# Performance work log

Hardware: AMD Instinct MI355X
Metric: run time of the kernel (lower is better)

## Reference

```python
import jax, jax.numpy as jnp
import numpy as np

N_HEAD = 16
N_EMBD = 1024
TIME_EMBD = 64
EPS = 1e-5

def _ln(x, w, b):
    mu = jnp.mean(x, axis=-1, keepdims=True)
    var = jnp.mean(jnp.square(x - mu), axis=-1, keepdims=True)
    return (x - mu) * jax.lax.rsqrt(var + EPS) * w + b

def _gelu(x):
    return jax.nn.gelu(x, approximate=False)

def setup_inputs() -> dict:
    key = jax.random.key(0)
    ks = jax.random.split(key, 12)
    B, T, D, TE = 2, 2048, N_EMBD, TIME_EMBD
    C = D + TE  # 1088
    s = lambda fan_in: 1.0 / np.sqrt(fan_in)
    return {
        "z": jax.random.normal(ks[0], (B, T, D), jnp.float32),
        "t": jax.random.uniform(ks[1], (B,), jnp.float32),
        # time_mlp: Linear(1, TE) -> GELU -> Linear(TE, TE)
        "w_t1": jax.random.normal(ks[2], (1, TE), jnp.float32) * s(1),
        "b_t1": jnp.zeros((TE,), jnp.float32),
        "w_t2": jax.random.normal(ks[3], (TE, TE), jnp.float32) * s(TE),
        "b_t2": jnp.zeros((TE,), jnp.float32),
        # attention
        "ln_a_w": jnp.ones((C,), jnp.float32),
        "ln_a_b": jnp.zeros((C,), jnp.float32),
        "w_attn": jax.random.normal(ks[4], (C, 3 * D), jnp.float32) * s(C),
        "b_attn": jnp.zeros((3 * D,), jnp.float32),
        "w_proj": jax.random.normal(ks[5], (D, D), jnp.float32) * s(D),
        "b_proj": jnp.zeros((D,), jnp.float32),
        # mlp
        "ln_m_w": jnp.ones((C,), jnp.float32),
        "ln_m_b": jnp.zeros((C,), jnp.float32),
        "w_fc": jax.random.normal(ks[6], (C, 4 * D), jnp.float32) * s(C),
        "b_fc": jnp.zeros((4 * D,), jnp.float32),
        "w_fc2": jax.random.normal(ks[7], (4 * D, D), jnp.float32) * s(4 * D),
        "b_fc2": jnp.zeros((D,), jnp.float32),
    }

def reference(z, t, w_t1, b_t1, w_t2, b_t2, ln_a_w, ln_a_b, w_attn, b_attn,
              w_proj, b_proj, ln_m_w, ln_m_b, w_fc, b_fc, w_fc2, b_fc2):
    B, T, D = z.shape
    H, hd = N_HEAD, N_EMBD // N_HEAD
    # time embedding: [B, TE] broadcast over T
    t_emb = _gelu(t[:, None] @ w_t1 + b_t1) @ w_t2 + b_t2
    t_emb_bt = jnp.broadcast_to(t_emb[:, None, :], (B, T, TIME_EMBD))
    # --- attention with time-conditioned input ---
    zt = jnp.concatenate([z, t_emb_bt], axis=-1)            # [B,T,D+TE]
    x = _ln(zt, ln_a_w, ln_a_b)
    qkv = x @ w_attn + b_attn                               # [B,T,3D]
    q, k, v = jnp.split(qkv, 3, axis=-1)
    q = q.reshape(B, T, H, hd)
    k = k.reshape(B, T, H, hd)
    v = v.reshape(B, T, H, hd)
    att = jnp.einsum('bqhd,bkhd->bhqk', q, k) * (1.0 / np.sqrt(hd))
    mask = jnp.tril(jnp.ones((T, T), bool))
    att = jnp.where(mask, att, -jnp.inf)
    att = jax.nn.softmax(att, axis=-1)
    y = jnp.einsum('bhqk,bkhd->bqhd', att, v).reshape(B, T, D)
    h = y @ w_proj + b_proj                                 # [B,T,D]
    # --- mlp with time-conditioned input ---
    ht = jnp.concatenate([h, t_emb_bt], axis=-1)
    m = _ln(ht, ln_m_w, ln_m_b)
    dz = _gelu(m @ w_fc + b_fc) @ w_fc2 + b_fc2             # [B,T,D]
    return dz
```

## Files before the change

kernel.cpp:

```cpp
#include <hip/hip_runtime.h>
#include <stdint.h>
#include <math.h>

#define T_SEQ 2048
#define NHEAD 16
#define HD 64
#define DMODEL 1024
#define CDIM 1088
#define MROWS 4096

typedef uint16_t u16;
typedef __bf16 b8v __attribute__((ext_vector_type(8)));
typedef float f4v __attribute__((ext_vector_type(4)));

typedef __attribute__((address_space(3))) void lds_void;
typedef const __attribute__((address_space(1))) void glb_void;

#define GLL(g, l) __builtin_amdgcn_global_load_lds((glb_void*)(g), (lds_void*)(l), 16, 0, 0)

__device__ __forceinline__ float b2f(u16 u) {
  union { uint32_t i; float f; } c; c.i = ((uint32_t)u) << 16; return c.f;
}
__device__ __forceinline__ u16 f2b(float f) {
  union { float f; uint32_t i; } c; c.f = f;
  uint32_t x = c.i;
  return (u16)((x + 0x7fffu + ((x >> 16) & 1u)) >> 16);
}
__device__ __forceinline__ float gelu_f(float x) {
  float ax = fabsf(x);
  float xs = ax * 0.70710678118654752f;
  float t = __frcp_rn(1.0f + 0.3275911f * xs);
  float poly = ((((1.061405429f * t - 1.453152027f) * t + 1.421413741f) * t
                 - 0.284496736f) * t + 0.254829592f) * t;
  float e = __expf(-xs * xs);
  float er = 1.0f - poly * e;
  er = copysignf(er, x);
  return 0.5f * x * (1.0f + er);
}

__global__ void time_mlp_kernel(const float* __restrict__ t, const float* __restrict__ w1,
                                const float* __restrict__ b1, const float* __restrict__ w2,
                                const float* __restrict__ b2, float* __restrict__ temb) {
  __shared__ float h1[2][64];
  int tid = threadIdx.x;
  int b = tid >> 6, i = tid & 63;
  float tv = t[b];
  h1[b][i] = gelu_f(tv * w1[i] + b1[i]);
  __syncthreads();
  float acc = b2[i];
  for (int k = 0; k < 64; ++k) acc += h1[b][k] * w2[k * 64 + i];
  temb[b * 64 + i] = acc;
}

__global__ __launch_bounds__(256) void transpose_kernel(const float* __restrict__ src,
                                                        u16* __restrict__ dst,
                                                        int R, int C) {
  __shared__ u16 tile[32][33];
  int tx = threadIdx.x & 31, ty = threadIdx.x >> 5;
  int c0 = blockIdx.x * 32, r0 = blockIdx.y * 32;
#pragma unroll
  for (int i = 0; i < 4; ++i) {
    int r = ty + i * 8;
    tile[r][tx] = f2b(src[(size_t)(r0 + r) * C + c0 + tx]);
  }
  __syncthreads();
#pragma unroll
  for (int i = 0; i < 4; ++i) {
    int c = ty + i * 8;
    dst[(size_t)(c0 + c) * R + r0 + tx] = tile[tx][c];
  }
}

__global__ __launch_bounds__(256) void add4_kernel(const float4* __restrict__ a,
                                                   const float4* __restrict__ b,
                                                   const float4* __restrict__ c,
                                                   const float4* __restrict__ d,
                                                   float4* __restrict__ o, int n4) {
  int i = blockIdx.x * 256 + threadIdx.x;
  if (i < n4) {
    float4 x = a[i], y = b[i], z = c[i], w = d[i];
    o[i] = float4{x.x + y.x + z.x + w.x, x.y + y.y + z.y + w.y,
                  x.z + y.z + z.z + w.z, x.w + y.w + z.w + w.w};
  }
}

__global__ __launch_bounds__(256) void ln_concat_kernel(const float* __restrict__ zf,
                                                        const float* __restrict__ zf2,
                                                        const float* __restrict__ temb,
                                                        const float* __restrict__ w,
                                                        const float* __restrict__ bvec,
                                                        u16* __restrict__ xout,
                                                        int mode) {
  __shared__ float red[4];
  int row = blockIdx.x;
  int b = row / T_SEQ;
  int tid = threadIdx.x;
  float v[5];
  float sum = 0.f;
#pragma unroll
  for (int i = 0; i < 5; ++i) {
    int c = tid + i * 256;
    float val = 0.f;
    if (c < CDIM) {
      if (c < DMODEL) {
        size_t idx = (size_t)row * DMODEL + c;
        if (mode == 1) val = zf[idx];
        else val = zf[idx] + zf2[idx];
      } else {
        val = temb[b * 64 + (c - DMODEL)];
      }
    }
    v[i] = val;
    sum += val;
  }
#pragma unroll
  for (int off = 32; off; off >>= 1) sum += __shfl_xor(sum, off, 64);
  int wv = tid >> 6, ln = tid & 63;
  if (ln == 0) red[wv] = sum;
  __syncthreads();
  float mean = (red[0] + red[1] + red[2] + red[3]) * (1.0f / CDIM);
  __syncthreads();
  float sq = 0.f;
#pragma unroll
  for (int i = 0; i < 5; ++i) {
    int c = tid + i * 256;
    if (c < CDIM) { float d = v[i] - mean; sq += d * d; }
  }
#pragma unroll
  for (int off = 32; off; off >>= 1) sq += __shfl_xor(sq, off, 64);
  if (ln == 0) red[wv] = sq;
  __syncthreads();
  float inv = rsqrtf((red[0] + red[1] + red[2] + red[3]) * (1.0f / CDIM) + 1e-5f);
#pragma unroll
  for (int i = 0; i < 5; ++i) {
    int c = tid + i * 256;
    if (c < CDIM)
      xout[(size_t)row * CDIM + c] = f2b((v[i] - mean) * inv * w[c] + bvec[c]);
  }
}

__global__ __launch_bounds__(512, 2) void gemm256_kernel(
    const u16* __restrict__ A, const u16* __restrict__ Bt,
    const float* __restrict__ bias,
    void* __restrict__ c0, void* __restrict__ c1,
    void* __restrict__ c2, void* __restrict__ c3,
    int M, int N, int K, int k_tiles, int do_gelu, int out_f32) {
  __shared__ u16 As[2][256 * 64];
  __shared__ u16 Bs[2][256 * 64];
  const int tid = threadIdx.x;
  const int wave = tid >> 6, lane = tid & 63;
  const int wr = wave >> 2, wc = wave & 3;
  const int lrow = lane & 15, quad = lane >> 4;

  int nxy = gridDim.x * gridDim.y;
  int bid = blockIdx.y * gridDim.x + blockIdx.x;
  int cpx = nxy >> 3;
  int swz = (bid & 7) * cpx + (bid >> 3);
  int bx = swz % gridDim.x, by = swz / gridDim.x;
  const int m0 = bx * 256, n0 = by * 256;
  const int kz = blockIdx.z;
  const int kb = kz * k_tiles * 64;
  const int NT = k_tiles;

  const int sr = tid >> 3;
  const int sc = ((tid & 7) ^ ((tid >> 3) & 7)) * 8;
  const u16* gA = A + (size_t)(m0 + sr) * K + kb + sc;
  const u16* gB = Bt + (size_t)(n0 + sr) * K + kb + sc;

  f4v acc[8][4] = {};
  b8v bq[2][4];

  auto STAGE_A = [&](int t, int h) {
    const u16* g = gA + (size_t)(h * 128) * K + t * 64;
    u16* l = (u16*)As[t & 1] + h * 8192 + (wave << 9);
    GLL(g, l);
    GLL(g + (size_t)64 * K, l + 4096);
  };
  auto STAGE_B = [&](int t, int h) {
    const u16* g = gB + (size_t)(h * 128) * K + t * 64;
    u16* l = (u16*)Bs[t & 1] + h * 8192 + (wave << 9);
    GLL(g, l);
    GLL(g + (size_t)64 * K, l + 4096);
  };

  STAGE_A(0, 0); STAGE_B(0, 0); STAGE_B(0, 1);
  STAGE_A(0, 1);
  if (NT > 1) { STAGE_A(1, 0); STAGE_B(1, 0); STAGE_B(1, 1); }
  if (NT > 1) asm volatile("s_waitcnt vmcnt(8)" ::: "memory");
  else        asm volatile("s_waitcnt vmcnt(2)" ::: "memory");
  __builtin_amdgcn_s_barrier();

  for (int t = 0; t < NT; ++t) {
    const char* abase = (const char*)As[t & 1];
    const char* bbase = (const char*)Bs[t & 1];
    const int asw = (lrow & 7) << 4;
    b8v af[4];

#pragma unroll
    for (int j = 0; j < 4; ++j)
      af[j] = *(const b8v*)(abase + (j * 32 + wr * 16 + lrow) * 128 + ((quad * 16) ^ asw));
#pragma unroll
    for (int n = 0; n < 4; ++n)
      bq[0][n] = *(const b8v*)(bbase + (wc * 64 + n * 16 + lrow) * 128 + ((quad * 16) ^ asw));
    if (t + 1 < NT) STAGE_A(t + 1, 1);
    __builtin_amdgcn_s_barrier();
    __builtin_amdgcn_s_setprio(1);
#pragma unroll
    for (int j = 0; j < 4; ++j)
#pragma unroll
      for (int n = 0; n < 4; ++n)
        acc[j][n] = __builtin_amdgcn_mfma_f32_16x16x32_bf16(bq[0][n], af[j], acc[j][n], 0, 0, 0);
    __builtin_amdgcn_s_setprio(0);
    __builtin_amdgcn_s_barrier();

#pragma unroll
    for (int j = 0; j < 4; ++j)
      af[j] = *(const b8v*)(abase + (j * 32 + wr * 16 + lrow) * 128 + ((64 + quad * 16) ^ asw));
#pragma unroll
    for (int n = 0; n < 4; ++n)
      bq[1][n] = *(const b8v*)(bbase + (wc * 64 + n * 16 + lrow) * 128 + ((64 + quad * 16) ^ asw));
    __builtin_amdgcn_s_barrier();
    __builtin_amdgcn_s_setprio(1);
#pragma unroll
    for (int j = 0; j < 4; ++j)
#pragma unroll
      for (int n = 0; n < 4; ++n)
        acc[j][n] = __builtin_amdgcn_mfma_f32_16x16x32_bf16(bq[1][n], af[j], acc[j][n], 0, 0, 0);
    __builtin_amdgcn_s_setprio(0);
    if (t + 1 < NT) asm volatile("s_waitcnt vmcnt(8)" ::: "memory");
    else            asm volatile("s_waitcnt vmcnt(0)" ::: "memory");
    __builtin_amdgcn_s_barrier();

#pragma unroll
    for (int j = 0; j < 4; ++j)
      af[j] = *(const b8v*)(abase + (128 + j * 32 + wr * 16 + lrow) * 128 + ((quad * 16) ^ asw));
    if (t + 2 < NT) { STAGE_B(t + 2, 0); STAGE_A(t + 2, 0); }
    __builtin_amdgcn_s_barrier();
    __builtin_amdgcn_s_setprio(1);
#pragma unroll
    for (int j = 0; j < 4; ++j)
#pragma unroll
      for (int n = 0; n < 4; ++n)
        acc[4 + j][n] = __builtin_amdgcn_mfma_f32_16x16x32_bf16(bq[0][n], af[j], acc[4 + j][n], 0, 0, 0);
    __builtin_amdgcn_s_setprio(0);
    __builtin_amdgcn_s_barrier();

#pragma unroll
    for (int j = 0; j < 4; ++j)
      af[j] = *(const b8v*)(abase + (128 + j * 32 + wr * 16 + lrow) * 128 + ((64 + quad * 16) ^ asw));
    if (t + 2 < NT) STAGE_B(t + 2, 1);
    __builtin_amdgcn_s_barrier();
    __builtin_amdgcn_s_setprio(1);
#pragma unroll
    for (int j = 0; j < 4; ++j)
#pragma unroll
      for (int n = 0; n < 4; ++n)
        acc[4 + j][n] = __builtin_amdgcn_mfma_f32_16x16x32_bf16(bq[1][n], af[j], acc[4 + j][n], 0, 0, 0);
    __builtin_amdgcn_s_setprio(0);
    if (t + 1 < NT) {
      if (t + 2 < NT) asm volatile("s_waitcnt vmcnt(8)" ::: "memory");
      else            asm volatile("s_waitcnt vmcnt(2)" ::: "memory");
    }
    __builtin_amdgcn_s_barrier();
  }

  void* Cout = (kz == 0) ? c0 : (kz == 1) ? c1 : (kz == 2) ? c2 : c3;
#pragma unroll
  for (int mh = 0; mh < 2; ++mh)
#pragma unroll
    for (int j = 0; j < 4; ++j) {
      int grow = m0 + mh * 128 + j * 32 + wr * 16 + lrow;
      size_t rb = (size_t)grow * N;
#pragma unroll
      for (int n = 0; n < 4; ++n) {
        int gcol = n0 + wc * 64 + n * 16 + quad * 4;
        float b0 = 0.f, b1 = 0.f, b2 = 0.f, b3 = 0.f;
        if (kz == 0) {
          float4 bv = *(const float4*)(bias + gcol);
          b0 = bv.x; b1 = bv.y; b2 = bv.z; b3 = bv.w;
        }
        f4v a = acc[mh * 4 + j][n];
        float v0 = a[0] + b0, v1 = a[1] + b1, v2 = a[2] + b2, v3 = a[3] + b3;
        if (do_gelu) {
          v0 = gelu_f(v0); v1 = gelu_f(v1); v2 = gelu_f(v2); v3 = gelu_f(v3);
        }
        if (out_f32) {
          *(float4*)((float*)Cout + rb + gcol) = float4{v0, v1, v2, v3};
        } else {
          ushort4 ov;
          ov.x = f2b(v0); ov.y = f2b(v1); ov.z = f2b(v2); ov.w = f2b(v3);
          *(ushort4*)((u16*)Cout + rb + gcol) = ov;
        }
      }
    }
}

__global__ __launch_bounds__(256) void gemm_splitk2_kernel(const u16* __restrict__ A,
                                                           const u16* __restrict__ Bt,
                                                           const float* __restrict__ bias,
                                                           float* __restrict__ C0,
                                                           float* __restrict__ C1,
                                                           int M, int N, int K, int Kc) {
  __shared__ u16 As[2][128 * 32];
  __shared__ u16 Bs[2][128 * 32];
  const int tid = threadIdx.x;
  const int wave = tid >> 6, lane = tid & 63;
  const int wr = wave >> 1, wc = wave & 1;
  const int m0 = blockIdx.x * 128;
  const int n0 = blockIdx.y * 128;
  const int kz = blockIdx.z;
  const int lrow = lane & 15, quad = lane >> 4;
  const int srow = lane >> 2, sseg = lane & 3;

  const u16* gA0 = A  + (size_t)(m0 + wave * 32 + srow) * K + kz * Kc + sseg * 8;
  const u16* gA1 = gA0 + (size_t)16 * K;
  const u16* gB0 = Bt + (size_t)(n0 + wave * 32 + srow) * K + kz * Kc + sseg * 8;
  const u16* gB1 = gB0 + (size_t)16 * K;
  const int la0 = (wave * 32) * 32, la1 = (wave * 32 + 16) * 32;

  f4v acc[4][4] = {};

  GLL(gA0, &As[0][la0]); GLL(gA1, &As[0][la1]);
  GLL(gB0, &Bs[0][la0]); GLL(gB1, &Bs[0][la1]);

  int cur = 0;
  for (int k0 = 0; k0 < Kc; k0 += 32) {
    __syncthreads();
    if (k0 + 32 < Kc) {
      int nxt = cur ^ 1;
      GLL(gA0 + k0 + 32, &As[nxt][la0]); GLL(gA1 + k0 + 32, &As[nxt][la1]);
      GLL(gB0 + k0 + 32, &Bs[nxt][la0]); GLL(gB1 + k0 + 32, &Bs[nxt][la1]);
    }
    b8v af[4], bfr[4];
#pragma unroll
    for (int mi = 0; mi < 4; ++mi)
      af[mi] = *(const b8v*)(&As[cur][(wr * 64 + mi * 16 + lrow) * 32 + quad * 8]);
#pragma unroll
    for (int ni = 0; ni < 4; ++ni)
      bfr[ni] = *(const b8v*)(&Bs[cur][(wc * 64 + ni * 16 + lrow) * 32 + quad * 8]);
#pragma unroll
    for (int mi = 0; mi < 4; ++mi)
#pragma unroll
      for (int ni = 0; ni < 4; ++ni)
        acc[mi][ni] = __builtin_amdgcn_mfma_f32_16x16x32_bf16(bfr[ni], af[mi], acc[mi][ni], 0, 0, 0);
    cur ^= 1;
  }

  float* C = kz ? C1 : C0;
#pragma unroll
  for (int mi = 0; mi < 4; ++mi) {
    int grow = m0 + wr * 64 + mi * 16 + lrow;
    size_t rb = (size_t)grow * N;
#pragma unroll
    for (int ni = 0; ni < 4; ++ni) {
      int gcol = n0 + wc * 64 + ni * 16 + quad * 4;
      float b0 = 0.f, b1 = 0.f, b2 = 0.f, b3 = 0.f;
      if (kz == 0) {
        float4 bv = *(const float4*)(bias + gcol);
        b0 = bv.x; b1 = bv.y; b2 = bv.z; b3 = bv.w;
      }
      *(float4*)(C + rb + gcol) = float4{acc[mi][ni][0] + b0, acc[mi][ni][1] + b1,
                                         acc[mi][ni][2] + b2, acc[mi][ni][3] + b3};
    }
  }
}

__global__ __launch_bounds__(256) void attn_mfma_kernel(const u16* __restrict__ qkv,
                                                        u16* __restrict__ y) {
  __shared__ u16 Ks[64 * 72];
  __shared__ u16 Vts[64 * 72];
  __shared__ u16 Ps[64 * 72];
  const int bh = blockIdx.x;
  const int b = bh >> 4, h = bh & 15;
  const int qt = 31 - blockIdx.y;
  const int tid = threadIdx.x, w = tid >> 6, lane = tid & 63;
  const int lrow = lane & 15, quad = lane >> 4;
  const int q0 = qt * 64;
  const int qg = q0 + w * 16 + lrow;

  b8v qf[2];
#pragma unroll
  for (int dc = 0; dc < 2; ++dc)
    qf[dc] = *(const b8v*)(qkv + (size_t)(b * T_SEQ + qg) * 3072 + h * 64 + dc * 32 + quad * 8);

  f4v oacc[4] = {};
  float mrun = -__builtin_inff(), lrun = 0.f;

  const int nch = qt + 1;
  for (int ct = 0; ct < nch; ++ct) {
    __syncthreads();
    {
      int r = tid >> 2, sg = tid & 3;
      const u16* src = qkv + (size_t)(b * T_SEQ + ct * 64 + r) * 3072 + h * 64 + 1024 + sg * 16;
      *(uint4*)(&Ks[r * 72 + sg * 16]) = *(const uint4*)(src);
      *(uint4*)(&Ks[r * 72 + sg * 16 + 8]) = *(const uint4*)(src + 8);
    }
    {
      int pr = tid >> 3, dsg = tid & 7;
      const u16* v0 = qkv + (size_t)(b * T_SEQ + ct * 64 + 2 * pr) * 3072 + h * 64 + 2048 + dsg * 8;
      uint4 a = *(const uint4*)(v0);
      uint4 bb = *(const uint4*)(v0 + 3072);
      uint32_t aw[4] = {a.x, a.y, a.z, a.w};
      uint32_t bw[4] = {bb.x, bb.y, bb.z, bb.w};
#pragma unroll
      for (int j = 0; j < 8; ++j) {
        int d = dsg * 8 + j;
        u16 ae = (u16)(aw[j >> 1] >> ((j & 1) * 16));
        u16 be = (u16)(bw[j >> 1] >> ((j & 1) * 16));
        int keyp = (2 * pr) ^ (((d >> 3) & 7) * 8);
        *(uint32_t*)(&Vts[d * 72 + keyp]) = (uint32_t)ae | ((uint32_t)be << 16);
      }
    }
    __syncthreads();

    f4v sacc[4] = {};
#pragma unroll
    for (int ks = 0; ks < 4; ++ks)
#pragma unroll
      for (int dc = 0; dc < 2; ++dc) {
        b8v kf = *(const b8v*)(&Ks[(ks * 16 + lrow) * 72 + dc * 32 + quad * 8]);
        sacc[ks] = __builtin_amdgcn_mfma_f32_16x16x32_bf16(kf, qf[dc], sacc[ks], 0, 0, 0);
      }

    bool diag = (ct == qt);
#pragma unroll
    for (int ks = 0; ks < 4; ++ks)
#pragma unroll
      for (int r = 0; r < 4; ++r) {
        float v = sacc[ks][r] * 0.125f;
        int key = ct * 64 + ks * 16 + quad * 4 + r;
        if (diag && key > qg) v = -__builtin_inff();
        sacc[ks][r] = v;
      }

    float rmax = sacc[0][0];
#pragma unroll
    for (int ks = 0; ks < 4; ++ks)
#pragma unroll
      for (int r = 0; r < 4; ++r) rmax = fmaxf(rmax, sacc[ks][r]);
    rmax = fmaxf(rmax, __shfl_xor(rmax, 16, 64));
    rmax = fmaxf(rmax, __shfl_xor(rmax, 32, 64));
    float mn = fmaxf(mrun, rmax);
    float al = __expf(mrun - mn);
    mrun = mn;
    float psum = 0.f;
#pragma unroll
    for (int ks = 0; ks < 4; ++ks)
#pragma unroll
      for (int r = 0; r < 4; ++r) {
        float p = __expf(sacc[ks][r] - mn);
        sacc[ks][r] = p;
        psum += p;
      }
    psum += __shfl_xor(psum, 16, 64);
    psum += __shfl_xor(psum, 32, 64);
    lrun = lrun * al + psum;
#pragma unroll
    for (int ds = 0; ds < 4; ++ds) oacc[ds] *= al;

#pragma unroll
    for (int ks = 0; ks < 4; ++ks) {
      ushort4 pw;
      pw.x = f2b(sacc[ks][0]); pw.y = f2b(sacc[ks][1]);
      pw.z = f2b(sacc[ks][2]); pw.w = f2b(sacc[ks][3]);
      *(ushort4*)(&Ps[(w * 16 + lrow) * 72 + ks * 16 + quad * 4]) = pw;
    }

    b8v pf[2];
#pragma unroll
    for (int kc = 0; kc < 2; ++kc)
      pf[kc] = *(const b8v*)(&Ps[(w * 16 + lrow) * 72 + kc * 32 + quad * 8]);
#pragma unroll
    for (int ds = 0; ds < 4; ++ds)
#pragma unroll
      for (int kc = 0; kc < 2; ++kc) {
        int d = ds * 16 + lrow;
        int off = (kc * 32 + quad * 8) ^ (((d >> 3) & 7) * 8);
        b8v vfv = *(const b8v*)(&Vts[d * 72 + off]);
        oacc[ds] = __builtin_amdgcn_mfma_f32_16x16x32_bf16(vfv, pf[kc], oacc[ds], 0, 0, 0);
      }
  }

  float rinv = 1.0f / lrun;
  u16* yrow = y + (size_t)(b * T_SEQ + qg) * DMODEL + h * 64;
#pragma unroll
  for (int ds = 0; ds < 4; ++ds) {
    ushort4 ov;
    ov.x = f2b(oacc[ds][0] * rinv);
    ov.y = f2b(oacc[ds][1] * rinv);
    ov.z = f2b(oacc[ds][2] * rinv);
    ov.w = f2b(oacc[ds][3] * rinv);
    *(ushort4*)(yrow + ds * 16 + quad * 4) = ov;
  }
}

extern "C" void kernel_launch(void* const* d_in, const int* in_sizes, int n_in,
                              void* d_out, int out_size, void* d_ws, size_t ws_size,
                              hipStream_t stream) {
  const float* z      = (const float*)d_in[0];
  const float* t      = (const float*)d_in[1];
  const float* w_t1   = (const float*)d_in[2];
  const float* b_t1   = (const float*)d_in[3];
  const float* w_t2   = (const float*)d_in[4];
  const float* b_t2   = (const float*)d_in[5];
  const float* ln_a_w = (const float*)d_in[6];
  const float* ln_a_b = (const float*)d_in[7];
  const float* w_attn = (const float*)d_in[8];
  const float* b_attn = (const float*)d_in[9];
  const float* w_proj = (const float*)d_in[10];
  const float* b_proj = (const float*)d_in[11];
  const float* ln_m_w = (const float*)d_in[12];
  const float* ln_m_b = (const float*)d_in[13];
  const float* w_fc   = (const float*)d_in[14];
  const float* b_fc   = (const float*)d_in[15];
  const float* w_fc2  = (const float*)d_in[16];
  const float* b_fc2  = (const float*)d_in[17];

  char* ws = (char*)d_ws;
  float* temb  = (float*)ws;
  u16* wT_attn = (u16*)(ws + 1024);
  u16* wT_proj = wT_attn + (size_t)3072 * 1088;
  u16* wT_fc   = wT_proj + (size_t)1024 * 1024;
  u16* wT_fc2  = wT_fc   + (size_t)4096 * 1088;
  u16* xbuf    = wT_fc2  + (size_t)1024 * 4096;
  u16* big     = xbuf    + (size_t)4096 * 1088;
  u16* ybuf    = big     + (size_t)4096 * 4096;
  float* p0    = (float*)(ybuf + (size_t)4096 * 1024);
  float* p1    = p0 + (size_t)4096 * 1024;
  float* p3    = (float*)wT_attn;

  time_mlp_kernel<<<dim3(1), dim3(128), 0, stream>>>(t, w_t1, b_t1, w_t2, b_t2, temb);

  transpose_kernel<<<dim3(3072 / 32, 1088 / 32), dim3(256), 0, stream>>>(w_attn, wT_attn, 1088, 3072);
  transpose_kernel<<<dim3(1024 / 32, 1024 / 32), dim3(256), 0, stream>>>(w_proj, wT_proj, 1024, 1024);
  transpose_kernel<<<dim3(4096 / 32, 1088 / 32), dim3(256), 0, stream>>>(w_fc, wT_fc, 1088, 4096);
  transpose_kernel<<<dim3(1024 / 32, 4096 / 32), dim3(256), 0, stream>>>(w_fc2, wT_fc2, 4096, 1024);

  ln_concat_kernel<<<dim3(MROWS), dim3(256), 0, stream>>>(
      z, (const float*)nullptr, temb, ln_a_w, ln_a_b, xbuf, 1);

  gemm256_kernel<<<dim3(16, 12, 1), dim3(512), 0, stream>>>(
      xbuf, wT_attn, b_attn, big, nullptr, nullptr, nullptr,
      MROWS, 3072, 1088, 17, 0, 0);

  attn_mfma_kernel<<<dim3(32, 32), dim3(256), 0, stream>>>(big, ybuf);

  gemm_splitk2_kernel<<<dim3(MROWS / 128, 1024 / 128, 2), dim3(256), 0, stream>>>(
      ybuf, wT_proj, b_proj, p0, p1, MROWS, 1024, 1024, 512);

  ln_concat_kernel<<<dim3(MROWS), dim3(256), 0, stream>>>(
      p0, p1, temb, ln_m_w, ln_m_b, xbuf, 2);

  gemm256_kernel<<<dim3(16, 16, 1), dim3(512), 0, stream>>>(
      xbuf, wT_fc, b_fc, big, nullptr, nullptr, nullptr,
      MROWS, 4096, 1088, 17, 1, 0);

  gemm256_kernel<<<dim3(16, 4, 4), dim3(512), 0, stream>>>(
      big, wT_fc2, b_fc2, p0, p1, d_out, p3,
      MROWS, 1024, 4096, 16, 0, 1);

  add4_kernel<<<dim3(MROWS * 1024 / 4 / 256), dim3(256), 0, stream>>>(
      (const float4*)p0, (const float4*)p1, (const float4*)d_out, (const float4*)p3,
      (float4*)d_out, MROWS * 1024 / 4);
}
```

Before: 384.8 us.

## Use 128-query attention tiles with shared K/V loads, exp2 softmax, packed bf16 conversion

The attention kernel now processes 128 query rows per block with 8 waves, so each K/V chunk loaded into LDS serves twice as many queries and the number of blocks is halved. Waves in the lower 64-row half skip compute on the final chunk but still take part in loading it. Softmax is folded into exp2 with a pre-multiplied log2e/sqrt(d) scale, and fp32-to-bf16 conversion uses the hardware packed convert instruction instead of manual rounding. The V transpose is rewritten with byte permutes and narrower loads. The trade-offs are fewer blocks for occupancy and idle waves on the diagonal chunk.

```diff
diff --git a/kernel.cpp b/kernel.cpp
--- a/kernel.cpp
+++ b/kernel.cpp
@@ -25,6 +25,14 @@
   union { float f; uint32_t i; } c; c.f = f;
   uint32_t x = c.i;
   return (u16)((x + 0x7fffu + ((x >> 16) & 1u)) >> 16);
+}
+__device__ __forceinline__ uint32_t cvt_pk_bf16(float lo, float hi) {
+  uint32_t r;
+  asm("v_cvt_pk_bf16_f32 %0, %1, %2" : "=v"(r) : "v"(lo), "v"(hi));
+  return r;
+}
+__device__ __forceinline__ float exp2_hw(float x) {
+  return __builtin_amdgcn_exp2f(x);
 }
 __device__ __forceinline__ float gelu_f(float x) {
   float ax = fabsf(x);
@@ -365,18 +373,19 @@
   }
 }
 
-__global__ __launch_bounds__(256) void attn_mfma_kernel(const u16* __restrict__ qkv,
+__global__ __launch_bounds__(512) void attn_mfma_kernel(const u16* __restrict__ qkv,
                                                         u16* __restrict__ y) {
   __shared__ u16 Ks[64 * 72];
   __shared__ u16 Vts[64 * 72];
-  __shared__ u16 Ps[64 * 72];
+  __shared__ u16 Ps[128 * 72];
   const int bh = blockIdx.x;
   const int b = bh >> 4, h = bh & 15;
-  const int qt = 31 - blockIdx.y;
+  const int qt = 15 - (int)blockIdx.y;
   const int tid = threadIdx.x, w = tid >> 6, lane = tid & 63;
   const int lrow = lane & 15, quad = lane >> 4;
-  const int q0 = qt * 64;
+  const int q0 = qt * 128;
   const int qg = q0 + w * 16 + lrow;
+  const int dchunk = 2 * qt + (w >> 2);
 
   b8v qf[2];
 #pragma unroll
@@ -385,33 +394,31 @@
 
   f4v oacc[4] = {};
   float mrun = -__builtin_inff(), lrun = 0.f;
-
-  const int nch = qt + 1;
+  const float SC = 0.18033688011112042f;
+
+  const int nch = 2 * qt + 2;
   for (int ct = 0; ct < nch; ++ct) {
     __syncthreads();
     {
-      int r = tid >> 2, sg = tid & 3;
-      const u16* src = qkv + (size_t)(b * T_SEQ + ct * 64 + r) * 3072 + h * 64 + 1024 + sg * 16;
-      *(uint4*)(&Ks[r * 72 + sg * 16]) = *(const uint4*)(src);
-      *(uint4*)(&Ks[r * 72 + sg * 16 + 8]) = *(const uint4*)(src + 8);
+      int r = tid >> 3, sg = tid & 7;
+      const u16* src = qkv + (size_t)(b * T_SEQ + ct * 64 + r) * 3072 + h * 64 + 1024 + sg * 8;
+      *(uint4*)(&Ks[r * 72 + sg * 8]) = *(const uint4*)(src);
     }
     {
-      int pr = tid >> 3, dsg = tid & 7;
-      const u16* v0 = qkv + (size_t)(b * T_SEQ + ct * 64 + 2 * pr) * 3072 + h * 64 + 2048 + dsg * 8;
-      uint4 a = *(const uint4*)(v0);
-      uint4 bb = *(const uint4*)(v0 + 3072);
-      uint32_t aw[4] = {a.x, a.y, a.z, a.w};
-      uint32_t bw[4] = {bb.x, bb.y, bb.z, bb.w};
-#pragma unroll
-      for (int j = 0; j < 8; ++j) {
-        int d = dsg * 8 + j;
-        u16 ae = (u16)(aw[j >> 1] >> ((j & 1) * 16));
-        u16 be = (u16)(bw[j >> 1] >> ((j & 1) * 16));
-        int keyp = (2 * pr) ^ (((d >> 3) & 7) * 8);
-        *(uint32_t*)(&Vts[d * 72 + keyp]) = (uint32_t)ae | ((uint32_t)be << 16);
-      }
+      int pr = tid >> 4, half = (tid >> 3) & 1, dsg = tid & 7;
+      int d0 = dsg * 8 + half * 4;
+      const u16* v0 = qkv + (size_t)(b * T_SEQ + ct * 64 + 2 * pr) * 3072 + h * 64 + 2048 + d0;
+      uint2 a = *(const uint2*)(v0);
+      uint2 bb = *(const uint2*)(v0 + 3072);
+      int keyp = (2 * pr) ^ (dsg * 8);
+      u16* vb = &Vts[d0 * 72 + keyp];
+      *(uint32_t*)(vb)           = __builtin_amdgcn_perm(bb.x, a.x, 0x05040100u);
+      *(uint32_t*)(vb + 72)      = __builtin_amdgcn_perm(bb.x, a.x, 0x07060302u);
+      *(uint32_t*)(vb + 144)     = __builtin_amdgcn_perm(bb.y, a.y, 0x05040100u);
+      *(uint32_t*)(vb + 216)     = __builtin_amdgcn_perm(bb.y, a.y, 0x07060302u);
     }
     __syncthreads();
+    if (ct > dchunk) continue;
 
     f4v sacc[4] = {};
 #pragma unroll
@@ -422,16 +429,15 @@
         sacc[ks] = __builtin_amdgcn_mfma_f32_16x16x32_bf16(kf, qf[dc], sacc[ks], 0, 0, 0);
       }
 
-    bool diag = (ct == qt);
-#pragma unroll
-    for (int ks = 0; ks < 4; ++ks)
-#pragma unroll
-      for (int r = 0; r < 4; ++r) {
-        float v = sacc[ks][r] * 0.125f;
-        int key = ct * 64 + ks * 16 + quad * 4 + r;
-        if (diag && key > qg) v = -__builtin_inff();
-        sacc[ks][r] = v;
-      }
+    if (ct == dchunk) {
+#pragma unroll
+      for (int ks = 0; ks < 4; ++ks)
+#pragma unroll
+        for (int r = 0; r < 4; ++r) {
+          int key = ct * 64 + ks * 16 + quad * 4 + r;
+          if (key > qg) sacc[ks][r] = -__builtin_inff();
+        }
+    }
 
     float rmax = sacc[0][0];
 #pragma unroll
@@ -440,31 +446,28 @@
       for (int r = 0; r < 4; ++r) rmax = fmaxf(rmax, sacc[ks][r]);
     rmax = fmaxf(rmax, __shfl_xor(rmax, 16, 64));
     rmax = fmaxf(rmax, __shfl_xor(rmax, 32, 64));
+    rmax *= SC;
     float mn = fmaxf(mrun, rmax);
-    float al = __expf(mrun - mn);
+    float al = exp2_hw(mrun - mn);
     mrun = mn;
     float psum = 0.f;
 #pragma unroll
-    for (int ks = 0; ks < 4; ++ks)
-#pragma unroll
-      for (int r = 0; r < 4; ++r) {
-        float p = __expf(sacc[ks][r] - mn);
-        sacc[ks][r] = p;
-        psum += p;
-      }
+    for (int ks = 0; ks < 4; ++ks) {
+      float p0 = exp2_hw(fmaf(sacc[ks][0], SC, -mn));
+      float p1 = exp2_hw(fmaf(sacc[ks][1], SC, -mn));
+      float p2 = exp2_hw(fmaf(sacc[ks][2], SC, -mn));
+      float p3 = exp2_hw(fmaf(sacc[ks][3], SC, -mn));
+      psum += (p0 + p1) + (p2 + p3);
+      uint2 pw;
+      pw.x = cvt_pk_bf16(p0, p1);
+      pw.y = cvt_pk_bf16(p2, p3);
+      *(uint2*)(&Ps[(w * 16 + lrow) * 72 + ks * 16 + quad * 4]) = pw;
+    }
     psum += __shfl_xor(psum, 16, 64);
     psum += __shfl_xor(psum, 32, 64);
     lrun = lrun * al + psum;
 #pragma unroll
     for (int ds = 0; ds < 4; ++ds) oacc[ds] *= al;
-
-#pragma unroll
-    for (int ks = 0; ks < 4; ++ks) {
-      ushort4 pw;
-      pw.x = f2b(sacc[ks][0]); pw.y = f2b(sacc[ks][1]);
-      pw.z = f2b(sacc[ks][2]); pw.w = f2b(sacc[ks][3]);
-      *(ushort4*)(&Ps[(w * 16 + lrow) * 72 + ks * 16 + quad * 4]) = pw;
-    }
 
     b8v pf[2];
 #pragma unroll
@@ -485,12 +488,10 @@
   u16* yrow = y + (size_t)(b * T_SEQ + qg) * DMODEL + h * 64;
 #pragma unroll
   for (int ds = 0; ds < 4; ++ds) {
-    ushort4 ov;
-    ov.x = f2b(oacc[ds][0] * rinv);
-    ov.y = f2b(oacc[ds][1] * rinv);
-    ov.z = f2b(oacc[ds][2] * rinv);
-    ov.w = f2b(oacc[ds][3] * rinv);
-    *(ushort4*)(yrow + ds * 16 + quad * 4) = ov;
+    uint2 ov;
+    ov.x = cvt_pk_bf16(oacc[ds][0] * rinv, oacc[ds][1] * rinv);
+    ov.y = cvt_pk_bf16(oacc[ds][2] * rinv, oacc[ds][3] * rinv);
+    *(uint2*)(yrow + ds * 16 + quad * 4) = ov;
   }
 }
 
@@ -543,7 +544,7 @@
       xbuf, wT_attn, b_attn, big, nullptr, nullptr, nullptr,
       MROWS, 3072, 1088, 17, 0, 0);
 
-  attn_mfma_kernel<<<dim3(32, 32), dim3(256), 0, stream>>>(big, ybuf);
+  attn_mfma_kernel<<<dim3(32, 16), dim3(512), 0, stream>>>(big, ybuf);
 
   gemm_splitk2_kernel<<<dim3(MROWS / 128, 1024 / 128, 2), dim3(256), 0, stream>>>(
       ybuf, wT_proj, b_proj, p0, p1, MROWS, 1024, 1024, 512);
```

Result: no change. 385.7 us (+0.2%).
